# Kernel tuning notes

Measured on AMD Instinct MI355X. Metric: run time of the kernel, lower is better.

The kernel has to match this reference:

```python
import jax, jax.numpy as jnp
import numpy as np

B, S, H, F, E, TOPK = 2, 1024, 1024, 2816, 8, 2

def setup_inputs() -> dict:
    key = jax.random.key(0)
    k1, k2, k3, k4 = jax.random.split(key, 4)
    return {
        "hidden_states": jax.random.normal(k1, (B, S, H), dtype=jnp.float32),
        "gate_w": jax.random.normal(k2, (E, H), dtype=jnp.float32) * 0.02,  # gate 1x1 conv == [E,H] matrix
        "w1": jax.random.normal(k3, (E, F, H), dtype=jnp.float32) * 0.02,   # per-expert up-proj
        "w2": jax.random.normal(k4, (E, H, F), dtype=jnp.float32) * 0.02,   # per-expert down-proj
        "top_k": TOPK,
    }

def reference(hidden_states, gate_w, w1, w2, top_k):
    b, s, h = hidden_states.shape
    e = gate_w.shape[0]
    x = hidden_states.reshape(-1, h)                       # [N, H]
    n = x.shape[0]
    # Router: 1x1 conv gate == linear, softmax, top-k, renormalize
    logits = x @ gate_w.T                                  # [N, E]
    probs = jax.nn.softmax(logits, axis=-1)
    topw, topi = jax.lax.top_k(probs, top_k)               # [N, k]
    topw = topw / jnp.sum(topw, axis=-1, keepdims=True)
    # Per-(token, expert) combine weight; zero for non-selected experts.
    # Equivalent to torch.where(topk_indices == e, topk_weights, 0).sum(-1).
    comb = jnp.zeros((n, e), dtype=x.dtype).at[jnp.arange(n)[:, None], topi].add(topw)  # [N, E]
    # Expert MLPs (1x1 convs == GEMMs): up -> SiLU -> down, weighted combine.
    up = jnp.einsum('nh,efh->nef', x, w1)                  # [N, E, F]
    act = jax.nn.silu(up)
    out = jnp.einsum('nef,ehf->neh', act, w2)              # [N, E, H]
    y = jnp.einsum('ne,neh->nh', comb, out)                # weighted combine
    return y.reshape(b, s, h)
```

## Files before the change

### kernel.cpp

```cpp
#include <hip/hip_runtime.h>
#include <hip/hip_bf16.h>
#include <stdint.h>

#define N_TOK 2048
#define H_DIM 1024
#define F_DIM 2816
#define N_EXP 8

#define BK 64
#define LDA 72

typedef __attribute__((ext_vector_type(8))) short bf16x8;
typedef __attribute__((ext_vector_type(4))) float f32x4;

static __device__ __forceinline__ unsigned short f2bf(float f) {
    union { float f; unsigned u; } v; v.f = f;
    unsigned r = v.u + 0x7fffu + ((v.u >> 16) & 1u);
    return (unsigned short)(r >> 16);
}

__global__ __launch_bounds__(256) void router_kernel(
    const float* __restrict__ x, const float* __restrict__ gate_w,
    int* __restrict__ counts, int* __restrict__ row_token, float* __restrict__ row_weight,
    int* __restrict__ slot_e, int* __restrict__ slot_pos)
{
    __shared__ float gsm[N_EXP * H_DIM];
    for (int i = threadIdx.x; i < N_EXP * H_DIM; i += 256) gsm[i] = gate_w[i];
    __syncthreads();

    const int wave = threadIdx.x >> 6;
    const int lane = threadIdx.x & 63;
    const int n = blockIdx.x * 4 + wave;
    if (n >= N_TOK) return;

    float xv[16];
#pragma unroll
    for (int i = 0; i < 16; i++) xv[i] = x[(size_t)n * H_DIM + lane + 64 * i];

    float logit[N_EXP];
#pragma unroll
    for (int e = 0; e < N_EXP; e++) {
        float p = 0.f;
#pragma unroll
        for (int i = 0; i < 16; i++) p += xv[i] * gsm[e * H_DIM + lane + 64 * i];
#pragma unroll
        for (int s = 32; s > 0; s >>= 1) p += __shfl_xor(p, s, 64);
        logit[e] = p;
    }

    if (lane == 0) {
        int e0 = 0; float l0 = logit[0];
#pragma unroll
        for (int e = 1; e < N_EXP; e++) if (logit[e] > l0) { l0 = logit[e]; e0 = e; }
        int e1 = -1; float l1 = -3.4e38f;
#pragma unroll
        for (int e = 0; e < N_EXP; e++) if (e != e0 && logit[e] > l1) { l1 = logit[e]; e1 = e; }
        float w0 = 1.f / (1.f + __expf(l1 - l0));
        float w1 = 1.f - w0;
        int p0 = atomicAdd(&counts[e0], 1);
        int p1 = atomicAdd(&counts[e1], 1);
        row_token[e0 * N_TOK + p0] = n;  row_weight[e0 * N_TOK + p0] = w0;
        row_token[e1 * N_TOK + p1] = n;  row_weight[e1 * N_TOK + p1] = w1;
        slot_e[n * 2 + 0] = e0;  slot_pos[n * 2 + 0] = p0;
        slot_e[n * 2 + 1] = e1;  slot_pos[n * 2 + 1] = p1;
    }
}

__global__ void scan_kernel(const int* __restrict__ counts, int* __restrict__ offsets)
{
    if (threadIdx.x == 0 && blockIdx.x == 0) {
        int acc = 0;
        for (int e = 0; e < N_EXP; e++) { offsets[e] = acc; acc += counts[e]; }
    }
}

__global__ __launch_bounds__(256) void up_gemm_kernel(
    const float* __restrict__ x, const float* __restrict__ w1,
    const int* __restrict__ counts, const int* __restrict__ offsets,
    const int* __restrict__ row_token,
    unsigned short* __restrict__ act)
{
    const int e = blockIdx.z;
    const int cnt = counts[e];
    const int mTile = blockIdx.y;
    if (mTile * 128 >= cnt) return;
    const int fTile = blockIdx.x;
    const int off = offsets[e];

    __shared__ __align__(16) unsigned short As[128 * LDA];
    __shared__ __align__(16) unsigned short Bs[128 * LDA];

    const int tid = threadIdx.x;
    const int lane = tid & 63;
    const int wave = tid >> 6;
    const int wm = (wave >> 1) * 64, wn = (wave & 1) * 64;

    int tokens[8];
#pragma unroll
    for (int j = 0; j < 8; j++) {
        int i = tid + 256 * j;
        int row = i >> 4;
        int pos = mTile * 128 + row;
        tokens[j] = row_token[e * N_TOK + min(pos, cnt - 1)];
    }

    f32x4 acc[4][4];
#pragma unroll
    for (int i = 0; i < 4; i++)
#pragma unroll
        for (int j = 0; j < 4; j++) acc[i][j] = (f32x4)(0.f);

    const float* wbase = w1 + (size_t)e * F_DIM * H_DIM + (size_t)(fTile * 128) * H_DIM;

    for (int kt = 0; kt < H_DIM / BK; kt++) {
        const int k0 = kt * BK;
#pragma unroll
        for (int j = 0; j < 8; j++) {
            int i = tid + 256 * j;
            int row = i >> 4, c = i & 15;
            const float4 v = *(const float4*)(x + (size_t)tokens[j] * H_DIM + k0 + c * 4);
            ushort4 b; b.x = f2bf(v.x); b.y = f2bf(v.y); b.z = f2bf(v.z); b.w = f2bf(v.w);
            *(ushort4*)(As + row * LDA + c * 4) = b;
        }
#pragma unroll
        for (int j = 0; j < 8; j++) {
            int i = tid + 256 * j;
            int row = i >> 4, c = i & 15;
            const float4 v = *(const float4*)(wbase + (size_t)row * H_DIM + k0 + c * 4);
            ushort4 b; b.x = f2bf(v.x); b.y = f2bf(v.y); b.z = f2bf(v.z); b.w = f2bf(v.w);
            *(ushort4*)(Bs + row * LDA + c * 4) = b;
        }
        __syncthreads();
#pragma unroll
        for (int ks = 0; ks < BK / 32; ks++) {
            const int kloc = ks * 32 + (lane >> 4) * 8;
            bf16x8 af[4], bfr[4];
#pragma unroll
            for (int i = 0; i < 4; i++)
                af[i] = *(const bf16x8*)(As + (wm + i * 16 + (lane & 15)) * LDA + kloc);
#pragma unroll
            for (int i = 0; i < 4; i++)
                bfr[i] = *(const bf16x8*)(Bs + (wn + i * 16 + (lane & 15)) * LDA + kloc);
#pragma unroll
            for (int i = 0; i < 4; i++)
#pragma unroll
                for (int j = 0; j < 4; j++)
                    acc[i][j] = __builtin_amdgcn_mfma_f32_16x16x32_bf16(af[i], bfr[j], acc[i][j], 0, 0, 0);
        }
        __syncthreads();
    }

#pragma unroll
    for (int i = 0; i < 4; i++) {
        const int mrow = wm + i * 16 + ((lane >> 4) << 2);
#pragma unroll
        for (int r = 0; r < 4; r++) {
            const int m = mTile * 128 + mrow + r;
            if (m < cnt) {
#pragma unroll
                for (int j = 0; j < 4; j++) {
                    float v = acc[i][j][r];
                    float s = v / (1.f + __expf(-v));
                    int col = fTile * 128 + wn + j * 16 + (lane & 15);
                    act[(size_t)(off + m) * F_DIM + col] = f2bf(s);
                }
            }
        }
    }
}

__global__ __launch_bounds__(256) void down_gemm_kernel(
    const unsigned short* __restrict__ act, const float* __restrict__ w2,
    const int* __restrict__ counts, const int* __restrict__ offsets,
    const float* __restrict__ row_weight,
    float* __restrict__ out_slot)
{
    const int e = blockIdx.z;
    const int cnt = counts[e];
    const int mTile = blockIdx.y;
    if (mTile * 128 >= cnt) return;
    const int hTile = blockIdx.x;
    const int off = offsets[e];

    __shared__ __align__(16) unsigned short As[128 * LDA];
    __shared__ __align__(16) unsigned short Bs[128 * LDA];

    const int tid = threadIdx.x;
    const int lane = tid & 63;
    const int wave = tid >> 6;
    const int wm = (wave >> 1) * 64, wn = (wave & 1) * 64;

    int rowsg[4];
#pragma unroll
    for (int j = 0; j < 4; j++) {
        int i = tid + 256 * j;
        int row = i >> 3;
        rowsg[j] = off + min(mTile * 128 + row, cnt - 1);
    }

    f32x4 acc[4][4];
#pragma unroll
    for (int i = 0; i < 4; i++)
#pragma unroll
        for (int j = 0; j < 4; j++) acc[i][j] = (f32x4)(0.f);

    const float* wbase = w2 + (size_t)e * H_DIM * F_DIM + (size_t)(hTile * 128) * F_DIM;

    for (int kt = 0; kt < F_DIM / BK; kt++) {
        const int k0 = kt * BK;
#pragma unroll
        for (int j = 0; j < 4; j++) {
            int i = tid + 256 * j;
            int row = i >> 3, c = i & 7;
            const uint4 v = *(const uint4*)(act + (size_t)rowsg[j] * F_DIM + k0 + c * 8);
            *(uint4*)(As + row * LDA + c * 8) = v;
        }
#pragma unroll
        for (int j = 0; j < 8; j++) {
            int i = tid + 256 * j;
            int row = i >> 4, c = i & 15;
            const float4 v = *(const float4*)(wbase + (size_t)row * F_DIM + k0 + c * 4);
            ushort4 b; b.x = f2bf(v.x); b.y = f2bf(v.y); b.z = f2bf(v.z); b.w = f2bf(v.w);
            *(ushort4*)(Bs + row * LDA + c * 4) = b;
        }
        __syncthreads();
#pragma unroll
        for (int ks = 0; ks < BK / 32; ks++) {
            const int kloc = ks * 32 + (lane >> 4) * 8;
            bf16x8 af[4], bfr[4];
#pragma unroll
            for (int i = 0; i < 4; i++)
                af[i] = *(const bf16x8*)(As + (wm + i * 16 + (lane & 15)) * LDA + kloc);
#pragma unroll
            for (int i = 0; i < 4; i++)
                bfr[i] = *(const bf16x8*)(Bs + (wn + i * 16 + (lane & 15)) * LDA + kloc);
#pragma unroll
            for (int i = 0; i < 4; i++)
#pragma unroll
                for (int j = 0; j < 4; j++)
                    acc[i][j] = __builtin_amdgcn_mfma_f32_16x16x32_bf16(af[i], bfr[j], acc[i][j], 0, 0, 0);
        }
        __syncthreads();
    }

#pragma unroll
    for (int i = 0; i < 4; i++) {
        const int mrow = wm + i * 16 + ((lane >> 4) << 2);
#pragma unroll
        for (int r = 0; r < 4; r++) {
            const int m = mTile * 128 + mrow + r;
            if (m < cnt) {
                const float w = row_weight[e * N_TOK + m];
#pragma unroll
                for (int j = 0; j < 4; j++) {
                    int col = hTile * 128 + wn + j * 16 + (lane & 15);
                    out_slot[(size_t)(off + m) * H_DIM + col] = w * acc[i][j][r];
                }
            }
        }
    }
}

__global__ __launch_bounds__(256) void combine_kernel(
    const float* __restrict__ out_slot, const int* __restrict__ offsets,
    const int* __restrict__ slot_e, const int* __restrict__ slot_pos,
    float* __restrict__ out)
{
    const int n = blockIdx.x;
    const int r0 = offsets[slot_e[n * 2 + 0]] + slot_pos[n * 2 + 0];
    const int r1 = offsets[slot_e[n * 2 + 1]] + slot_pos[n * 2 + 1];
    const int t = threadIdx.x;
    const float4 a = *(const float4*)(out_slot + (size_t)r0 * H_DIM + t * 4);
    const float4 b = *(const float4*)(out_slot + (size_t)r1 * H_DIM + t * 4);
    float4 c; c.x = a.x + b.x; c.y = a.y + b.y; c.z = a.z + b.z; c.w = a.w + b.w;
    *(float4*)(out + (size_t)n * H_DIM + t * 4) = c;
}

extern "C" void kernel_launch(void* const* d_in, const int* in_sizes, int n_in,
                              void* d_out, int out_size, void* d_ws, size_t ws_size,
                              hipStream_t stream) {
    const float* x      = (const float*)d_in[0];
    const float* gate_w = (const float*)d_in[1];
    const float* w1     = (const float*)d_in[2];
    const float* w2     = (const float*)d_in[3];
    float* out = (float*)d_out;

    char* ws = (char*)d_ws;
    size_t o = 0;
    auto alloc = [&](size_t bytes) -> void* {
        void* p = ws + o;
        o = (o + bytes + 255) & ~(size_t)255;
        return p;
    };
    int*   counts     = (int*)  alloc(N_EXP * sizeof(int));
    int*   offsets    = (int*)  alloc(N_EXP * sizeof(int));
    int*   row_token  = (int*)  alloc((size_t)N_EXP * N_TOK * sizeof(int));
    float* row_weight = (float*)alloc((size_t)N_EXP * N_TOK * sizeof(float));
    int*   slot_e     = (int*)  alloc((size_t)N_TOK * 2 * sizeof(int));
    int*   slot_pos   = (int*)  alloc((size_t)N_TOK * 2 * sizeof(int));
    unsigned short* act = (unsigned short*)alloc((size_t)N_TOK * 2 * F_DIM * sizeof(unsigned short));
    float* out_slot   = (float*)alloc((size_t)N_TOK * 2 * H_DIM * sizeof(float));

    hipMemsetAsync(counts, 0, N_EXP * sizeof(int), stream);

    router_kernel<<<N_TOK / 4, 256, 0, stream>>>(x, gate_w, counts, row_token, row_weight, slot_e, slot_pos);
    scan_kernel<<<1, 64, 0, stream>>>(counts, offsets);
    up_gemm_kernel<<<dim3(F_DIM / 128, N_TOK / 128, N_EXP), 256, 0, stream>>>(
        x, w1, counts, offsets, row_token, act);
    down_gemm_kernel<<<dim3(H_DIM / 128, N_TOK / 128, N_EXP), 256, 0, stream>>>(
        act, w2, counts, offsets, row_weight, out_slot);
    combine_kernel<<<N_TOK, 256, 0, stream>>>(out_slot, offsets, slot_e, slot_pos, out);
}
```

Baseline: 402.3 us.

## Pre-convert weights and activations to bf16, prefetch tiles, split-K the down GEMM

```diff
diff --git a/kernel.cpp b/kernel.cpp
--- a/kernel.cpp
+++ b/kernel.cpp
@@ -19,10 +19,29 @@
     return (unsigned short)(r >> 16);
 }
 
+#define WELEMS (N_EXP * F_DIM * H_DIM)
+#define CONV_BLOCKS (WELEMS / (256 * 16))
+__global__ __launch_bounds__(256) void convert_w_kernel(
+    const float* __restrict__ w1, const float* __restrict__ w2,
+    unsigned short* __restrict__ w1b, unsigned short* __restrict__ w2b)
+{
+    const float* src; unsigned short* dst; int blk;
+    if (blockIdx.x < CONV_BLOCKS) { src = w1; dst = w1b; blk = blockIdx.x; }
+    else                          { src = w2; dst = w2b; blk = blockIdx.x - CONV_BLOCKS; }
+    size_t base = (size_t)blk * (256 * 16) + threadIdx.x * 4;
+#pragma unroll
+    for (int j = 0; j < 4; j++) {
+        const float4 v = *(const float4*)(src + base + j * 1024);
+        ushort4 b; b.x = f2bf(v.x); b.y = f2bf(v.y); b.z = f2bf(v.z); b.w = f2bf(v.w);
+        *(ushort4*)(dst + base + j * 1024) = b;
+    }
+}
+
 __global__ __launch_bounds__(256) void router_kernel(
     const float* __restrict__ x, const float* __restrict__ gate_w,
     int* __restrict__ counts, int* __restrict__ row_token, float* __restrict__ row_weight,
-    int* __restrict__ slot_e, int* __restrict__ slot_pos)
+    int* __restrict__ slot_e, int* __restrict__ slot_pos,
+    unsigned short* __restrict__ xb)
 {
     __shared__ float gsm[N_EXP * H_DIM];
     for (int i = threadIdx.x; i < N_EXP * H_DIM; i += 256) gsm[i] = gate_w[i];
@@ -31,11 +50,12 @@
     const int wave = threadIdx.x >> 6;
     const int lane = threadIdx.x & 63;
     const int n = blockIdx.x * 4 + wave;
-    if (n >= N_TOK) return;
 
     float xv[16];
 #pragma unroll
     for (int i = 0; i < 16; i++) xv[i] = x[(size_t)n * H_DIM + lane + 64 * i];
+#pragma unroll
+    for (int i = 0; i < 16; i++) xb[(size_t)n * H_DIM + lane + 64 * i] = f2bf(xv[i]);
 
     float logit[N_EXP];
 #pragma unroll
@@ -75,7 +95,7 @@
 }
 
 __global__ __launch_bounds__(256) void up_gemm_kernel(
-    const float* __restrict__ x, const float* __restrict__ w1,
+    const unsigned short* __restrict__ xb, const unsigned short* __restrict__ w1b,
     const int* __restrict__ counts, const int* __restrict__ offsets,
     const int* __restrict__ row_token,
     unsigned short* __restrict__ act)
@@ -94,15 +114,12 @@
     const int lane = tid & 63;
     const int wave = tid >> 6;
     const int wm = (wave >> 1) * 64, wn = (wave & 1) * 64;
-
-    int tokens[8];
-#pragma unroll
-    for (int j = 0; j < 8; j++) {
-        int i = tid + 256 * j;
-        int row = i >> 4;
-        int pos = mTile * 128 + row;
-        tokens[j] = row_token[e * N_TOK + min(pos, cnt - 1)];
-    }
+    const int srow = tid >> 3, scol = (tid & 7) * 8;
+
+    int tokenA[4];
+#pragma unroll
+    for (int j = 0; j < 4; j++)
+        tokenA[j] = row_token[e * N_TOK + min(mTile * 128 + srow + 32 * j, cnt - 1)];
 
     f32x4 acc[4][4];
 #pragma unroll
@@ -110,27 +127,31 @@
 #pragma unroll
         for (int j = 0; j < 4; j++) acc[i][j] = (f32x4)(0.f);
 
-    const float* wbase = w1 + (size_t)e * F_DIM * H_DIM + (size_t)(fTile * 128) * H_DIM;
-
-    for (int kt = 0; kt < H_DIM / BK; kt++) {
+    const unsigned short* wbase = w1b + (size_t)e * F_DIM * H_DIM + (size_t)(fTile * 128 + srow) * H_DIM + scol;
+
+    uint4 ra[4], rb[4];
+    auto loadAB = [&](int kt) {
         const int k0 = kt * BK;
 #pragma unroll
-        for (int j = 0; j < 8; j++) {
-            int i = tid + 256 * j;
-            int row = i >> 4, c = i & 15;
-            const float4 v = *(const float4*)(x + (size_t)tokens[j] * H_DIM + k0 + c * 4);
-            ushort4 b; b.x = f2bf(v.x); b.y = f2bf(v.y); b.z = f2bf(v.z); b.w = f2bf(v.w);
-            *(ushort4*)(As + row * LDA + c * 4) = b;
-        }
-#pragma unroll
-        for (int j = 0; j < 8; j++) {
-            int i = tid + 256 * j;
-            int row = i >> 4, c = i & 15;
-            const float4 v = *(const float4*)(wbase + (size_t)row * H_DIM + k0 + c * 4);
-            ushort4 b; b.x = f2bf(v.x); b.y = f2bf(v.y); b.z = f2bf(v.z); b.w = f2bf(v.w);
-            *(ushort4*)(Bs + row * LDA + c * 4) = b;
-        }
+        for (int j = 0; j < 4; j++)
+            ra[j] = *(const uint4*)(xb + (size_t)tokenA[j] * H_DIM + k0 + scol);
+#pragma unroll
+        for (int j = 0; j < 4; j++)
+            rb[j] = *(const uint4*)(wbase + (size_t)(32 * j) * H_DIM + k0);
+    };
+    auto stage = [&] {
+#pragma unroll
+        for (int j = 0; j < 4; j++) *(uint4*)(As + (srow + 32 * j) * LDA + scol) = ra[j];
+#pragma unroll
+        for (int j = 0; j < 4; j++) *(uint4*)(Bs + (srow + 32 * j) * LDA + scol) = rb[j];
+    };
+
+    const int NKT = H_DIM / BK;
+    loadAB(0);
+    for (int kt = 0; kt < NKT; kt++) {
+        stage();
         __syncthreads();
+        if (kt + 1 < NKT) loadAB(kt + 1);
 #pragma unroll
         for (int ks = 0; ks < BK / 32; ks++) {
             const int kloc = ks * 32 + (lane >> 4) * 8;
@@ -170,12 +191,13 @@
 }
 
 __global__ __launch_bounds__(256) void down_gemm_kernel(
-    const unsigned short* __restrict__ act, const float* __restrict__ w2,
+    const unsigned short* __restrict__ act, const unsigned short* __restrict__ w2b,
     const int* __restrict__ counts, const int* __restrict__ offsets,
     const float* __restrict__ row_weight,
     float* __restrict__ out_slot)
 {
-    const int e = blockIdx.z;
+    const int e = blockIdx.z >> 1;
+    const int ksplit = blockIdx.z & 1;
     const int cnt = counts[e];
     const int mTile = blockIdx.y;
     if (mTile * 128 >= cnt) return;
@@ -189,14 +211,12 @@
     const int lane = tid & 63;
     const int wave = tid >> 6;
     const int wm = (wave >> 1) * 64, wn = (wave & 1) * 64;
-
-    int rowsg[4];
-#pragma unroll
-    for (int j = 0; j < 4; j++) {
-        int i = tid + 256 * j;
-        int row = i >> 3;
-        rowsg[j] = off + min(mTile * 128 + row, cnt - 1);
-    }
+    const int srow = tid >> 3, scol = (tid & 7) * 8;
+
+    int rowA[4];
+#pragma unroll
+    for (int j = 0; j < 4; j++)
+        rowA[j] = off + min(mTile * 128 + srow + 32 * j, cnt - 1);
 
     f32x4 acc[4][4];
 #pragma unroll
@@ -204,26 +224,32 @@
 #pragma unroll
         for (int j = 0; j < 4; j++) acc[i][j] = (f32x4)(0.f);
 
-    const float* wbase = w2 + (size_t)e * H_DIM * F_DIM + (size_t)(hTile * 128) * F_DIM;
-
-    for (int kt = 0; kt < F_DIM / BK; kt++) {
+    const unsigned short* wbase = w2b + (size_t)e * H_DIM * F_DIM + (size_t)(hTile * 128 + srow) * F_DIM + scol;
+
+    uint4 ra[4], rb[4];
+    auto loadAB = [&](int kt) {
         const int k0 = kt * BK;
 #pragma unroll
-        for (int j = 0; j < 4; j++) {
-            int i = tid + 256 * j;
-            int row = i >> 3, c = i & 7;
-            const uint4 v = *(const uint4*)(act + (size_t)rowsg[j] * F_DIM + k0 + c * 8);
-            *(uint4*)(As + row * LDA + c * 8) = v;
-        }
-#pragma unroll
-        for (int j = 0; j < 8; j++) {
-            int i = tid + 256 * j;
-            int row = i >> 4, c = i & 15;
-            const float4 v = *(const float4*)(wbase + (size_t)row * F_DIM + k0 + c * 4);
-            ushort4 b; b.x = f2bf(v.x); b.y = f2bf(v.y); b.z = f2bf(v.z); b.w = f2bf(v.w);
-            *(ushort4*)(Bs + row * LDA + c * 4) = b;
-        }
+        for (int j = 0; j < 4; j++)
+            ra[j] = *(const uint4*)(act + (size_t)rowA[j] * F_DIM + k0 + scol);
+#pragma unroll
+        for (int j = 0; j < 4; j++)
+            rb[j] = *(const uint4*)(wbase + (size_t)(32 * j) * F_DIM + k0);
+    };
+    auto stage = [&] {
+#pragma unroll
+        for (int j = 0; j < 4; j++) *(uint4*)(As + (srow + 32 * j) * LDA + scol) = ra[j];
+#pragma unroll
+        for (int j = 0; j < 4; j++) *(uint4*)(Bs + (srow + 32 * j) * LDA + scol) = rb[j];
+    };
+
+    const int KT_PER = (F_DIM / BK) / 2;
+    const int kt0 = ksplit * KT_PER;
+    loadAB(kt0);
+    for (int kt = kt0; kt < kt0 + KT_PER; kt++) {
+        stage();
         __syncthreads();
+        if (kt + 1 < kt0 + KT_PER) loadAB(kt + 1);
 #pragma unroll
         for (int ks = 0; ks < BK / 32; ks++) {
             const int kloc = ks * 32 + (lane >> 4) * 8;
@@ -243,6 +269,7 @@
         __syncthreads();
     }
 
+    float* slot = out_slot + (size_t)ksplit * (N_TOK * 2) * H_DIM;
 #pragma unroll
     for (int i = 0; i < 4; i++) {
         const int mrow = wm + i * 16 + ((lane >> 4) << 2);
@@ -254,7 +281,7 @@
 #pragma unroll
                 for (int j = 0; j < 4; j++) {
                     int col = hTile * 128 + wn + j * 16 + (lane & 15);
-                    out_slot[(size_t)(off + m) * H_DIM + col] = w * acc[i][j][r];
+                    slot[(size_t)(off + m) * H_DIM + col] = w * acc[i][j][r];
                 }
             }
         }
@@ -267,12 +294,19 @@
     float* __restrict__ out)
 {
     const int n = blockIdx.x;
-    const int r0 = offsets[slot_e[n * 2 + 0]] + slot_pos[n * 2 + 0];
-    const int r1 = offsets[slot_e[n * 2 + 1]] + slot_pos[n * 2 + 1];
+    const size_t r0 = offsets[slot_e[n * 2 + 0]] + slot_pos[n * 2 + 0];
+    const size_t r1 = offsets[slot_e[n * 2 + 1]] + slot_pos[n * 2 + 1];
+    const size_t KS = (size_t)(N_TOK * 2) * H_DIM;
     const int t = threadIdx.x;
-    const float4 a = *(const float4*)(out_slot + (size_t)r0 * H_DIM + t * 4);
-    const float4 b = *(const float4*)(out_slot + (size_t)r1 * H_DIM + t * 4);
-    float4 c; c.x = a.x + b.x; c.y = a.y + b.y; c.z = a.z + b.z; c.w = a.w + b.w;
+    const float4 a0 = *(const float4*)(out_slot + r0 * H_DIM + t * 4);
+    const float4 a1 = *(const float4*)(out_slot + KS + r0 * H_DIM + t * 4);
+    const float4 b0 = *(const float4*)(out_slot + r1 * H_DIM + t * 4);
+    const float4 b1 = *(const float4*)(out_slot + KS + r1 * H_DIM + t * 4);
+    float4 c;
+    c.x = (a0.x + a1.x) + (b0.x + b1.x);
+    c.y = (a0.y + a1.y) + (b0.y + b1.y);
+    c.z = (a0.z + a1.z) + (b0.z + b1.z);
+    c.w = (a0.w + a1.w) + (b0.w + b1.w);
     *(float4*)(out + (size_t)n * H_DIM + t * 4) = c;
 }
 
@@ -298,16 +332,20 @@
     float* row_weight = (float*)alloc((size_t)N_EXP * N_TOK * sizeof(float));
     int*   slot_e     = (int*)  alloc((size_t)N_TOK * 2 * sizeof(int));
     int*   slot_pos   = (int*)  alloc((size_t)N_TOK * 2 * sizeof(int));
+    unsigned short* xb  = (unsigned short*)alloc((size_t)N_TOK * H_DIM * sizeof(unsigned short));
     unsigned short* act = (unsigned short*)alloc((size_t)N_TOK * 2 * F_DIM * sizeof(unsigned short));
-    float* out_slot   = (float*)alloc((size_t)N_TOK * 2 * H_DIM * sizeof(float));
+    unsigned short* w1b = (unsigned short*)alloc((size_t)WELEMS * sizeof(unsigned short));
+    unsigned short* w2b = (unsigned short*)alloc((size_t)WELEMS * sizeof(unsigned short));
+    float* out_slot   = (float*)alloc((size_t)2 * N_TOK * 2 * H_DIM * sizeof(float));
 
     hipMemsetAsync(counts, 0, N_EXP * sizeof(int), stream);
 
-    router_kernel<<<N_TOK / 4, 256, 0, stream>>>(x, gate_w, counts, row_token, row_weight, slot_e, slot_pos);
+    convert_w_kernel<<<2 * CONV_BLOCKS, 256, 0, stream>>>(w1, w2, w1b, w2b);
+    router_kernel<<<N_TOK / 4, 256, 0, stream>>>(x, gate_w, counts, row_token, row_weight, slot_e, slot_pos, xb);
     scan_kernel<<<1, 64, 0, stream>>>(counts, offsets);
     up_gemm_kernel<<<dim3(F_DIM / 128, N_TOK / 128, N_EXP), 256, 0, stream>>>(
-        x, w1, counts, offsets, row_token, act);
-    down_gemm_kernel<<<dim3(H_DIM / 128, N_TOK / 128, N_EXP), 256, 0, stream>>>(
-        act, w2, counts, offsets, row_weight, out_slot);
+        xb, w1b, counts, offsets, row_token, act);
+    down_gemm_kernel<<<dim3(H_DIM / 128, N_TOK / 128, N_EXP * 2), 256, 0, stream>>>(
+        act, w2b, counts, offsets, row_weight, out_slot);
     combine_kernel<<<N_TOK, 256, 0, stream>>>(out_slot, offsets, slot_e, slot_pos, out);
 }
```

Result: slower. 617.8 us (+53.6%).
